# Performance work log

Measured on AMD Instinct MI355X. Metric: run time of the kernel, lower is better.

The kernel has to match this reference:

```python
import jax, jax.numpy as jnp
import numpy as np
import math

D_MODEL = 512
NUM_HEADS = 8
D_K = D_MODEL // NUM_HEADS
MAX_LEN = 500
BATCH = 32
SEQ = 480


def setup_inputs() -> dict:
    key = jax.random.key(0)
    ks = jax.random.split(key, 10)
    s = 0.02
    x = jax.random.normal(ks[0], (BATCH, SEQ, D_MODEL), dtype=jnp.float32)
    wq = jax.random.normal(ks[1], (D_MODEL, D_MODEL), dtype=jnp.float32) * s
    bq = jnp.zeros((D_MODEL,), jnp.float32)
    wk = jax.random.normal(ks[2], (D_MODEL, D_MODEL), dtype=jnp.float32) * s
    bk = jnp.zeros((D_MODEL,), jnp.float32)
    wv = jax.random.normal(ks[3], (D_MODEL, D_MODEL), dtype=jnp.float32) * s
    bv = jnp.zeros((D_MODEL,), jnp.float32)
    wo = jax.random.normal(ks[4], (D_MODEL, D_MODEL), dtype=jnp.float32) * s
    bo = jnp.zeros((D_MODEL,), jnp.float32)
    rel_bias = jax.random.normal(ks[5], (NUM_HEADS, MAX_LEN, MAX_LEN), dtype=jnp.float32) * 0.02
    return {"x": x, "wq": wq, "bq": bq, "wk": wk, "bk": bk, "wv": wv,
            "bv": bv, "wo": wo, "bo": bo, "rel_bias": rel_bias}


def reference(x, wq, bq, wk, bk, wv, bv, wo, bo, rel_bias):
    B, S, D = x.shape
    H, dk = NUM_HEADS, D_K
    scale = math.sqrt(dk)
    # QKV projections -> [B, H, S, dk]
    q = (x @ wq + bq).reshape(B, S, H, dk).transpose(0, 2, 1, 3)
    k = (x @ wk + bk).reshape(B, S, H, dk).transpose(0, 2, 1, 3)
    v = (x @ wv + bv).reshape(B, S, H, dk).transpose(0, 2, 1, 3)
    scores = jnp.einsum('bhqd,bhkd->bhqk', q, k) / scale
    scores = scores + rel_bias[None, :, :S, :S]
    causal = jnp.triu(jnp.ones((S, S), dtype=bool), k=1)  # True where j > i
    scores = jnp.where(causal[None, None], -jnp.inf, scores)
    attn = jax.nn.softmax(scores, axis=-1)
    ctx = jnp.einsum('bhqk,bhkd->bhqd', attn, v)
    ctx = ctx.transpose(0, 2, 1, 3).reshape(B, S, D)
    out = ctx @ wo + bo
    return out, attn.mean(axis=1)
```

## Files before the change

### kernel.cpp

```cpp
#include <hip/hip_runtime.h>
#include <hip/hip_bf16.h>


typedef unsigned short ushort_t;
typedef __attribute__((ext_vector_type(8))) short short8;
typedef __attribute__((ext_vector_type(4))) float floatx4;
typedef __attribute__((ext_vector_type(2))) __fp16 half2v;

#define NB 32
#define NS 480
#define ND 512
#define NH 8
#define NDK 64
#define MAXLEN 500
#define PSTR 36
#define SCL 0.18033688f

__device__ __forceinline__ ushort_t f2bf(float f) {
  union { float f; unsigned u; } v; v.f = f;
  unsigned r = v.u + 0x7FFFu + ((v.u >> 16) & 1u);
  return (ushort_t)(r >> 16);
}

#define GLOAD_LDS16(g, l)                                                      \
  __builtin_amdgcn_global_load_lds(                                            \
      (const __attribute__((address_space(1))) void*)(g),                      \
      (__attribute__((address_space(3))) void*)(l), 16, 0, 0)

__global__ __launch_bounds__(256)
void cvt_xw(const float* __restrict__ x, const float* __restrict__ wq,
            const float* __restrict__ wk, const float* __restrict__ wv,
            const float* __restrict__ wo, ushort_t* __restrict__ xb,
            ushort_t* __restrict__ wqT, ushort_t* __restrict__ wkT,
            ushort_t* __restrict__ wvT, ushort_t* __restrict__ woT) {
  __shared__ float t[32][33];
  const int bid = blockIdx.x;
  if (bid < 7680) {
    int idx = bid * 256 + threadIdx.x;
    float4 v = ((const float4*)x)[idx];
    ushort4 o;
    o.x = f2bf(v.x); o.y = f2bf(v.y); o.z = f2bf(v.z); o.w = f2bf(v.w);
    ((ushort4*)xb)[idx] = o;
    return;
  }
  const int q = bid - 7680;
  const int z = q >> 8;
  const float* w = (z == 0) ? wq : (z == 1) ? wk : (z == 2) ? wv : wo;
  ushort_t* wT = (z == 0) ? wqT : (z == 1) ? wkT : (z == 2) ? wvT : woT;
  int k0 = (q & 15) * 32, n0 = ((q >> 4) & 15) * 32;
  int tx = threadIdx.x & 31, ty = threadIdx.x >> 5;
#pragma unroll
  for (int yy = 0; yy < 4; ++yy)
    t[ty + yy * 8][tx] = w[(k0 + ty + yy * 8) * ND + n0 + tx];
  __syncthreads();
#pragma unroll
  for (int yy = 0; yy < 4; ++yy)
    wT[(n0 + ty + yy * 8) * ND + k0 + tx] = f2bf(t[tx][ty + yy * 8]);
}

__global__ void cvt_rbt(const float* __restrict__ rel_bias, float* __restrict__ rbt) {
  int kt = blockIdx.x, ib = blockIdx.y, h = blockIdx.z;
  int lm = threadIdx.x & 15, ii = threadIdx.x >> 4;
  int i = ib * 16 + ii;
  float f0 = rel_bias[((size_t)h * MAXLEN + i) * MAXLEN + kt * 32 + lm] * 1.44269504f;
  float f1 = rel_bias[((size_t)h * MAXLEN + i) * MAXLEN + kt * 32 + 16 + lm] * 1.44269504f;
  float2 o = {f0, f1};
  *(float2*)&rbt[(((size_t)h * 15 + kt) * NS + i) * 32 + 2 * lm] = o;
}

__global__ __launch_bounds__(256)
void qkv_gemm(const ushort_t* __restrict__ xb,
              const ushort_t* __restrict__ wqT, const ushort_t* __restrict__ wkT,
              const ushort_t* __restrict__ wvT,
              const float* __restrict__ bq, const float* __restrict__ bk,
              const float* __restrict__ bv,
              ushort_t* __restrict__ qb, ushort_t* __restrict__ kb,
              ushort_t* __restrict__ vtil) {
  __shared__ __align__(16) ushort_t sA[128 * 64];
  __shared__ __align__(16) ushort_t sB[128 * 64];
  const int tid = threadIdx.x;
  const int wid = tid >> 6, lane = tid & 63;
  const int lm = lane & 15, quad = lane >> 4;
  const int wr = wid >> 1, wc = wid & 1;
  const int z = blockIdx.z;

  floatx4 zero4 = {0.f, 0.f, 0.f, 0.f};
  floatx4 acc[4][4];
#pragma unroll
  for (int i = 0; i < 4; ++i)
#pragma unroll
    for (int j = 0; j < 4; ++j) acc[i][j] = zero4;

  if (z < 2) {
    if (blockIdx.x >= 120) return;
    const int row0 = blockIdx.x * 128;
    const int col0 = blockIdx.y * 128;
    const ushort_t* Bt = (z == 0) ? wqT : wkT;
    const float* bias = (z == 0) ? bq : bk;

    for (int k0 = 0; k0 < ND; k0 += 64) {
#pragma unroll
      for (int c = 0; c < 4; ++c) {
        int li = c * 256 + tid;
        int row = li >> 3, kc = li & 7;
        int kcs = kc ^ (row & 7);
        GLOAD_LDS16(xb + (row0 + row) * ND + k0 + kcs * 8, sA + (c * 256 + wid * 64) * 8);
        GLOAD_LDS16(Bt + (col0 + row) * ND + k0 + kcs * 8, sB + (c * 256 + wid * 64) * 8);
      }
      __syncthreads();
#pragma unroll
      for (int h2 = 0; h2 < 2; ++h2) {
        short8 a[4], b[4];
#pragma unroll
        for (int i = 0; i < 4; ++i) {
          int row = wr * 64 + i * 16 + lm;
          a[i] = *(const short8*)&sA[row * 64 + (((h2 << 2) | quad) ^ (lm & 7)) * 8];
        }
#pragma unroll
        for (int j = 0; j < 4; ++j) {
          int row = wc * 64 + j * 16 + lm;
          b[j] = *(const short8*)&sB[row * 64 + (((h2 << 2) | quad) ^ (lm & 7)) * 8];
        }
#pragma unroll
        for (int i = 0; i < 4; ++i)
#pragma unroll
          for (int j = 0; j < 4; ++j)
            acc[i][j] = __builtin_amdgcn_mfma_f32_16x16x32_bf16(a[i], b[j], acc[i][j], 0, 0, 0);
      }
      __syncthreads();
    }

    float bsv[4];
#pragma unroll
    for (int j = 0; j < 4; ++j) bsv[j] = bias[col0 + wc * 64 + j * 16 + lm];

#pragma unroll
    for (int i = 0; i < 4; ++i)
#pragma unroll
      for (int j = 0; j < 4; ++j)
#pragma unroll
        for (int r = 0; r < 4; ++r) {
          int m = row0 + wr * 64 + i * 16 + quad * 4 + r;
          int n = col0 + wc * 64 + j * 16 + lm;
          float val = acc[i][j][r] + bsv[j];
          int bb = m / NS, s = m - bb * NS;
          int h = n >> 6, d = n & 63;
          ushort_t o = f2bf(val);
          if (z == 0) qb[((bb * NH + h) * NS + s) * NDK + d] = o;
          else        kb[((bb * NH + h) * NS + s) * NDK + d] = o;
        }
  } else {
    const int b = blockIdx.x >> 2;
    const int row0 = (blockIdx.x & 3) * 128;
    const int col0 = blockIdx.y * 128;
    const ushort_t* xbb = xb + (size_t)b * NS * ND;

    for (int k0 = 0; k0 < ND; k0 += 64) {
#pragma unroll
      for (int c = 0; c < 4; ++c) {
        int li = c * 256 + tid;
        int row = li >> 3, kc = li & 7;
        int kcs = kc ^ (row & 7);
        GLOAD_LDS16(wvT + (row0 + row) * ND + k0 + kcs * 8, sA + (c * 256 + wid * 64) * 8);
        int srow = min(col0 + row, NS - 1);
        GLOAD_LDS16(xbb + srow * ND + k0 + kcs * 8, sB + (c * 256 + wid * 64) * 8);
      }
      __syncthreads();
#pragma unroll
      for (int h2 = 0; h2 < 2; ++h2) {
        short8 a[4], b2[4];
#pragma unroll
        for (int i = 0; i < 4; ++i) {
          int row = wr * 64 + i * 16 + lm;
          a[i] = *(const short8*)&sA[row * 64 + (((h2 << 2) | quad) ^ (lm & 7)) * 8];
        }
#pragma unroll
        for (int j = 0; j < 4; ++j) {
          int row = wc * 64 + j * 16 + lm;
          b2[j] = *(const short8*)&sB[row * 64 + (((h2 << 2) | quad) ^ (lm & 7)) * 8];
        }
#pragma unroll
        for (int i = 0; i < 4; ++i)
#pragma unroll
          for (int j = 0; j < 4; ++j)
            acc[i][j] = __builtin_amdgcn_mfma_f32_16x16x32_bf16(a[i], b2[j], acc[i][j], 0, 0, 0);
      }
      __syncthreads();
    }

#pragma unroll
    for (int i = 0; i < 4; ++i)
#pragma unroll
      for (int r = 0; r < 4; ++r) {
        int m = row0 + wr * 64 + i * 16 + quad * 4 + r;
        float bias = bv[m];
#pragma unroll
        for (int j = 0; j < 4; ++j) {
          int n = col0 + wc * 64 + j * 16 + lm;
          if (n < NS) {
            size_t idx = (((size_t)b * NH + (m >> 6)) * 15 + (n >> 5)) * 2048 +
                         (m & 63) * 32 + (n & 31);
            vtil[idx] = f2bf(acc[i][j][r] + bias);
          }
        }
      }
  }
}

__global__ __launch_bounds__(256)
void flash_attn(const ushort_t* __restrict__ qb, const ushort_t* __restrict__ kb,
                const ushort_t* __restrict__ vtil, const float* __restrict__ rbt,
                ushort_t* __restrict__ ctxb, float* __restrict__ cst,
                uint4* __restrict__ pscr) {
  const int bh = blockIdx.x;
  const int b = bh >> 3, h = bh & 7;
  const int tid = threadIdx.x;
  const int wid = tid >> 6, lane = tid & 63;
  const int lm = lane & 15, quad = lane >> 4;

  __shared__ __align__(16) ushort_t sP[4][32 * PSTR];

  const int slot = blockIdx.y * 4 + wid;
  const int tA = (slot == 7) ? 14 : slot;
  const int tB = (slot == 7) ? -1 : 13 - slot;

  const ushort_t* qh = qb + (size_t)bh * NS * NDK;
  const ushort_t* kh = kb + (size_t)bh * NS * NDK;
  const ushort_t* vb = vtil + (size_t)bh * 15 * 2048;
  const float* rb = rbt + (size_t)h * 15 * NS * 32;

#pragma unroll 1
  for (int ti = 0; ti < 2; ++ti) {
    const int t = (ti == 0) ? tA : tB;
    if (t < 0) break;
    const int nkt = t + 1;
    uint4* pp = pscr + ((size_t)(bh * 120 + (t * (t + 1)) / 2)) * 128 + lane;

    short8 aq[2][2];
#pragma unroll
    for (int g = 0; g < 2; ++g) {
      aq[g][0] = *(const short8*)&qh[(t * 32 + g * 16 + lm) * NDK + quad * 8];
      aq[g][1] = *(const short8*)&qh[(t * 32 + g * 16 + lm) * NDK + 32 + quad * 8];
    }

    float lsum[2][4];
    floatx4 O[2][4];
    floatx4 zero4 = {0.f, 0.f, 0.f, 0.f};
#pragma unroll
    for (int g = 0; g < 2; ++g) {
#pragma unroll
      for (int r = 0; r < 4; ++r) lsum[g][r] = 0.f;
#pragma unroll
      for (int jd = 0; jd < 4; ++jd) O[g][jd] = zero4;
    }

    for (int kt = 0; kt < nkt; ++kt) {
      const int kvA = kt * 32 + lm;
      const int kvB = kvA + 16;
      short8 bkA0 = *(const short8*)&kh[kvA * NDK + quad * 8];
      short8 bkA1 = *(const short8*)&kh[kvA * NDK + 32 + quad * 8];
      short8 bkB0 = *(const short8*)&kh[kvB * NDK + quad * 8];
      short8 bkB1 = *(const short8*)&kh[kvB * NDK + 32 + quad * 8];
      short8 bv2[4];
#pragma unroll
      for (int jd = 0; jd < 4; ++jd)
        bv2[jd] = *(const short8*)&vb[kt * 2048 + (jd * 16 + lm) * 32 + quad * 8];
      float2 bb[2][4];
#pragma unroll
      for (int g = 0; g < 2; ++g)
#pragma unroll
        for (int r = 0; r < 4; ++r) {
          int i = t * 32 + g * 16 + quad * 4 + r;
          bb[g][r] = *(const float2*)&rb[((size_t)kt * NS + i) * 32 + 2 * lm];
        }

      floatx4 sA[2], sB[2];
      __builtin_amdgcn_s_setprio(1);
#pragma unroll
      for (int g = 0; g < 2; ++g) {
        floatx4 s = zero4;
        s = __builtin_amdgcn_mfma_f32_16x16x32_bf16(aq[g][0], bkA0, s, 0, 0, 0);
        s = __builtin_amdgcn_mfma_f32_16x16x32_bf16(aq[g][1], bkA1, s, 0, 0, 0);
        sA[g] = s;
        s = zero4;
        s = __builtin_amdgcn_mfma_f32_16x16x32_bf16(aq[g][0], bkB0, s, 0, 0, 0);
        s = __builtin_amdgcn_mfma_f32_16x16x32_bf16(aq[g][1], bkB1, s, 0, 0, 0);
        sB[g] = s;
      }
      __builtin_amdgcn_s_setprio(0);

      const bool diag = (kt == t);
#pragma unroll
      for (int g = 0; g < 2; ++g) {
        unsigned pw[4];
#pragma unroll
        for (int r = 0; r < 4; ++r) {
          float p0 = __builtin_amdgcn_exp2f(fmaf(sA[g][r], SCL, bb[g][r].x));
          float p1 = __builtin_amdgcn_exp2f(fmaf(sB[g][r], SCL, bb[g][r].y));
          if (diag) {
            int i = t * 32 + g * 16 + quad * 4 + r;
            if (kvA > i) p0 = 0.f;
            if (kvB > i) p1 = 0.f;
          }
          lsum[g][r] += p0 + p1;
          unsigned pk;
          asm("v_cvt_pk_bf16_f32 %0, %1, %2" : "=v"(pk) : "v"(p0), "v"(p1));
          sP[wid][(g * 16 + quad * 4 + r) * PSTR + lm] = (ushort_t)(pk & 0xffffu);
          sP[wid][(g * 16 + quad * 4 + r) * PSTR + 16 + lm] = (ushort_t)(pk >> 16);
          half2v hp = __builtin_amdgcn_cvt_pkrtz(p0, p1);
          pw[r] = *(unsigned*)&hp;
        }
        uint4 pq = {pw[0], pw[1], pw[2], pw[3]};
        pp[(size_t)kt * 128 + g * 64] = pq;
      }

      __builtin_amdgcn_s_setprio(1);
#pragma unroll
      for (int g = 0; g < 2; ++g) {
        short8 ap = *(const short8*)&sP[wid][(g * 16 + lm) * PSTR + quad * 8];
#pragma unroll
        for (int jd = 0; jd < 4; ++jd)
          O[g][jd] = __builtin_amdgcn_mfma_f32_16x16x32_bf16(ap, bv2[jd], O[g][jd], 0, 0, 0);
      }
      __builtin_amdgcn_s_setprio(0);
    }

#pragma unroll
    for (int off = 1; off < 16; off <<= 1)
#pragma unroll
      for (int g = 0; g < 2; ++g)
#pragma unroll
        for (int r = 0; r < 4; ++r) lsum[g][r] += __shfl_xor(lsum[g][r], off, 64);

#pragma unroll
    for (int g = 0; g < 2; ++g) {
      float rinv[4];
#pragma unroll
      for (int r = 0; r < 4; ++r) rinv[r] = 1.f / lsum[g][r];
#pragma unroll
      for (int jd = 0; jd < 4; ++jd)
#pragma unroll
        for (int r = 0; r < 4; ++r) {
          int i = t * 32 + g * 16 + quad * 4 + r;
          ctxb[((size_t)b * NS + i) * ND + h * NDK + jd * 16 + lm] =
              f2bf(O[g][jd][r] * rinv[r]);
        }
      if (lm == 0) {
#pragma unroll
        for (int r = 0; r < 4; ++r) {
          int i = t * 32 + g * 16 + quad * 4 + r;
          cst[(size_t)bh * NS + i] = rinv[r];
        }
      }
    }
  }
}

__global__ __launch_bounds__(64)
void attn_mean_p(const uint4* __restrict__ pscr, const float* __restrict__ cst,
                 float* __restrict__ am) {
  const int b = blockIdx.x, t = blockIdx.y, kt = blockIdx.z;
  const int lane = threadIdx.x;
  const int lm = lane & 15, quad = lane >> 4;
  float* outp = am + ((size_t)b * NS + t * 32) * NS + (size_t)kt * 32;
  if (kt > t) {
#pragma unroll
    for (int g = 0; g < 2; ++g)
#pragma unroll
      for (int r = 0; r < 4; ++r) {
        int row = g * 16 + quad * 4 + r;
        outp[(size_t)row * NS + lm] = 0.f;
        outp[(size_t)row * NS + 16 + lm] = 0.f;
      }
    return;
  }
  const int m = (t * (t + 1)) / 2 + kt;
  float a0[2][4], a1[2][4];
#pragma unroll
  for (int g = 0; g < 2; ++g)
#pragma unroll
    for (int r = 0; r < 4; ++r) { a0[g][r] = 0.f; a1[g][r] = 0.f; }

#pragma unroll
  for (int h = 0; h < NH; ++h) {
    const uint4* pp = pscr + ((size_t)(b * NH + h) * 120 + m) * 128 + lane;
    uint4 q0 = pp[0];
    uint4 q1 = pp[64];
    unsigned pu[8] = {q0.x, q0.y, q0.z, q0.w, q1.x, q1.y, q1.z, q1.w};
    const float* cp = cst + (size_t)(b * NH + h) * NS + t * 32 + quad * 4;
    float4 rv0 = *(const float4*)cp;
    float4 rv1 = *(const float4*)(cp + 16);
    float rv[8] = {rv0.x, rv0.y, rv0.z, rv0.w, rv1.x, rv1.y, rv1.z, rv1.w};
#pragma unroll
    for (int g = 0; g < 2; ++g)
#pragma unroll
      for (int r = 0; r < 4; ++r) {
        half2v hp = *(half2v*)&pu[g * 4 + r];
        a0[g][r] = fmaf((float)hp.x, rv[g * 4 + r], a0[g][r]);
        a1[g][r] = fmaf((float)hp.y, rv[g * 4 + r], a1[g][r]);
      }
  }

#pragma unroll
  for (int g = 0; g < 2; ++g)
#pragma unroll
    for (int r = 0; r < 4; ++r) {
      int row = g * 16 + quad * 4 + r;
      outp[(size_t)row * NS + lm] = a0[g][r] * 0.125f;
      outp[(size_t)row * NS + 16 + lm] = a1[g][r] * 0.125f;
    }
}

__global__ __launch_bounds__(256)
void out_gemm(const ushort_t* __restrict__ ctxb, const ushort_t* __restrict__ woT,
              const float* __restrict__ bo, float* __restrict__ out) {
  __shared__ __align__(16) ushort_t sA[128 * 64];
  __shared__ __align__(16) ushort_t sB[128 * 64];
  const int tid = threadIdx.x;
  const int wid = tid >> 6, lane = tid & 63;
  const int lm = lane & 15, quad = lane >> 4;
  const int wr = wid >> 1, wc = wid & 1;
  const int row0 = blockIdx.x * 128;
  const int col0 = blockIdx.y * 128;

  floatx4 zero4 = {0.f, 0.f, 0.f, 0.f};
  floatx4 acc[4][4];
#pragma unroll
  for (int i = 0; i < 4; ++i)
#pragma unroll
    for (int j = 0; j < 4; ++j) acc[i][j] = zero4;

  for (int k0 = 0; k0 < ND; k0 += 64) {
#pragma unroll
    for (int c = 0; c < 4; ++c) {
      int li = c * 256 + tid;
      int row = li >> 3, kc = li & 7;
      int kcs = kc ^ (row & 7);
      GLOAD_LDS16(ctxb + (row0 + row) * ND + k0 + kcs * 8, sA + (c * 256 + wid * 64) * 8);
      GLOAD_LDS16(woT + (col0 + row) * ND + k0 + kcs * 8, sB + (c * 256 + wid * 64) * 8);
    }
    __syncthreads();
#pragma unroll
    for (int h2 = 0; h2 < 2; ++h2) {
      short8 a[4], b[4];
#pragma unroll
      for (int i = 0; i < 4; ++i) {
        int row = wr * 64 + i * 16 + lm;
        a[i] = *(const short8*)&sA[row * 64 + (((h2 << 2) | quad) ^ (lm & 7)) * 8];
      }
#pragma unroll
      for (int j = 0; j < 4; ++j) {
        int row = wc * 64 + j * 16 + lm;
        b[j] = *(const short8*)&sB[row * 64 + (((h2 << 2) | quad) ^ (lm & 7)) * 8];
      }
#pragma unroll
      for (int i = 0; i < 4; ++i)
#pragma unroll
        for (int j = 0; j < 4; ++j)
          acc[i][j] = __builtin_amdgcn_mfma_f32_16x16x32_bf16(a[i], b[j], acc[i][j], 0, 0, 0);
    }
    __syncthreads();
  }

  float bsv[4];
#pragma unroll
  for (int j = 0; j < 4; ++j) bsv[j] = bo[col0 + wc * 64 + j * 16 + lm];

#pragma unroll
  for (int i = 0; i < 4; ++i)
#pragma unroll
    for (int j = 0; j < 4; ++j)
#pragma unroll
      for (int r = 0; r < 4; ++r) {
        int m = row0 + wr * 64 + i * 16 + quad * 4 + r;
        int n = col0 + wc * 64 + j * 16 + lm;
        out[m * ND + n] = acc[i][j][r] + bsv[j];
      }
}

extern "C" void kernel_launch(void* const* d_in, const int* in_sizes, int n_in,
                              void* d_out, int out_size, void* d_ws, size_t ws_size,
                              hipStream_t stream) {
  const float* x  = (const float*)d_in[0];
  const float* wq = (const float*)d_in[1];
  const float* bq = (const float*)d_in[2];
  const float* wk = (const float*)d_in[3];
  const float* bk = (const float*)d_in[4];
  const float* wv = (const float*)d_in[5];
  const float* bv = (const float*)d_in[6];
  const float* wo = (const float*)d_in[7];
  const float* bo = (const float*)d_in[8];
  const float* rel_bias = (const float*)d_in[9];

  char* w = (char*)d_ws;
  ushort_t* xb  = (ushort_t*)w;
  ushort_t* wqT = (ushort_t*)(w + 15728640);
  ushort_t* wkT = wqT + 262144;
  ushort_t* wvT = wkT + 262144;
  ushort_t* woT = wvT + 262144;
  ushort_t* qb  = (ushort_t*)(w + 15728640 + 4 * 524288);
  ushort_t* kb  = qb + 7864320;
  ushort_t* vtil = kb + 7864320;
  ushort_t* ctxb = vtil + 7864320;
  float* cstat = (float*)(w + 80740352);
  uint4* pscr = (uint4*)(w + 81264640);
  float* rbt = (float*)w;

  float* out0 = (float*)d_out;
  float* attn_mean = out0 + 7864320;

  cvt_xw<<<dim3(8704), dim3(256), 0, stream>>>(x, wq, wk, wv, wo, xb, wqT, wkT, wvT, woT);
  qkv_gemm<<<dim3(128, 4, 3), dim3(256), 0, stream>>>(xb, wqT, wkT, wvT, bq, bk, bv,
                                                      qb, kb, vtil);
  cvt_rbt<<<dim3(15, 30, 8), dim3(256), 0, stream>>>(rel_bias, rbt);
  flash_attn<<<dim3(256, 2), dim3(256), 0, stream>>>(qb, kb, vtil, rbt, ctxb, cstat, pscr);
  attn_mean_p<<<dim3(32, 15, 15), dim3(64), 0, stream>>>(pscr, cstat, attn_mean);
  out_gemm<<<dim3(120, 4), dim3(256), 0, stream>>>(ctxb, woT, bo, out0);
}
```

Before: 226.4 us.

## Double-buffer LDS tiles in QKV and output GEMMs to overlap loads with MFMA

Allocates two LDS buffers per operand in the QKV and output projection GEMMs. The global-to-LDS load of the next K tile is issued before computing on the current one, leaving one barrier per iteration. This is meant to hide global load latency behind MFMA work. It doubles LDS use per block to 64 KB, which may lower occupancy.

```diff
diff --git a/kernel.cpp b/kernel.cpp
--- a/kernel.cpp
+++ b/kernel.cpp
@@ -76,8 +76,8 @@
               const float* __restrict__ bv,
               ushort_t* __restrict__ qb, ushort_t* __restrict__ kb,
               ushort_t* __restrict__ vtil) {
-  __shared__ __align__(16) ushort_t sA[128 * 64];
-  __shared__ __align__(16) ushort_t sB[128 * 64];
+  __shared__ __align__(16) ushort_t sA[2][128 * 64];
+  __shared__ __align__(16) ushort_t sB[2][128 * 64];
   const int tid = threadIdx.x;
   const int wid = tid >> 6, lane = tid & 63;
   const int lm = lane & 15, quad = lane >> 4;
@@ -90,6 +90,9 @@
   for (int i = 0; i < 4; ++i)
 #pragma unroll
     for (int j = 0; j < 4; ++j) acc[i][j] = zero4;
+
+  const int srow_ = tid >> 3, skc = tid & 7;
+  const int skcs = skc ^ (srow_ & 7);
 
   if (z < 2) {
     if (blockIdx.x >= 120) return;
@@ -98,28 +101,39 @@
     const ushort_t* Bt = (z == 0) ? wqT : wkT;
     const float* bias = (z == 0) ? bq : bk;
 
-    for (int k0 = 0; k0 < ND; k0 += 64) {
-#pragma unroll
-      for (int c = 0; c < 4; ++c) {
-        int li = c * 256 + tid;
-        int row = li >> 3, kc = li & 7;
-        int kcs = kc ^ (row & 7);
-        GLOAD_LDS16(xb + (row0 + row) * ND + k0 + kcs * 8, sA + (c * 256 + wid * 64) * 8);
-        GLOAD_LDS16(Bt + (col0 + row) * ND + k0 + kcs * 8, sB + (c * 256 + wid * 64) * 8);
-      }
-      __syncthreads();
+#pragma unroll
+    for (int c = 0; c < 4; ++c) {
+      int row = c * 32 + srow_;
+      GLOAD_LDS16(xb + (row0 + row) * ND + skcs * 8, &sA[0][(c * 256 + wid * 64) * 8]);
+      GLOAD_LDS16(Bt + (col0 + row) * ND + skcs * 8, &sB[0][(c * 256 + wid * 64) * 8]);
+    }
+    __syncthreads();
+
+    int buf = 0;
+    for (int t = 0; t < 8; ++t) {
+      if (t < 7) {
+        int k0n = (t + 1) * 64;
+#pragma unroll
+        for (int c = 0; c < 4; ++c) {
+          int row = c * 32 + srow_;
+          GLOAD_LDS16(xb + (row0 + row) * ND + k0n + skcs * 8,
+                      &sA[buf ^ 1][(c * 256 + wid * 64) * 8]);
+          GLOAD_LDS16(Bt + (col0 + row) * ND + k0n + skcs * 8,
+                      &sB[buf ^ 1][(c * 256 + wid * 64) * 8]);
+        }
+      }
 #pragma unroll
       for (int h2 = 0; h2 < 2; ++h2) {
         short8 a[4], b[4];
 #pragma unroll
         for (int i = 0; i < 4; ++i) {
           int row = wr * 64 + i * 16 + lm;
-          a[i] = *(const short8*)&sA[row * 64 + (((h2 << 2) | quad) ^ (lm & 7)) * 8];
+          a[i] = *(const short8*)&sA[buf][row * 64 + (((h2 << 2) | quad) ^ (lm & 7)) * 8];
         }
 #pragma unroll
         for (int j = 0; j < 4; ++j) {
           int row = wc * 64 + j * 16 + lm;
-          b[j] = *(const short8*)&sB[row * 64 + (((h2 << 2) | quad) ^ (lm & 7)) * 8];
+          b[j] = *(const short8*)&sB[buf][row * 64 + (((h2 << 2) | quad) ^ (lm & 7)) * 8];
         }
 #pragma unroll
         for (int i = 0; i < 4; ++i)
@@ -128,6 +142,7 @@
             acc[i][j] = __builtin_amdgcn_mfma_f32_16x16x32_bf16(a[i], b[j], acc[i][j], 0, 0, 0);
       }
       __syncthreads();
+      buf ^= 1;
     }
 
     float bsv[4];
@@ -155,29 +170,41 @@
     const int col0 = blockIdx.y * 128;
     const ushort_t* xbb = xb + (size_t)b * NS * ND;
 
-    for (int k0 = 0; k0 < ND; k0 += 64) {
-#pragma unroll
-      for (int c = 0; c < 4; ++c) {
-        int li = c * 256 + tid;
-        int row = li >> 3, kc = li & 7;
-        int kcs = kc ^ (row & 7);
-        GLOAD_LDS16(wvT + (row0 + row) * ND + k0 + kcs * 8, sA + (c * 256 + wid * 64) * 8);
-        int srow = min(col0 + row, NS - 1);
-        GLOAD_LDS16(xbb + srow * ND + k0 + kcs * 8, sB + (c * 256 + wid * 64) * 8);
-      }
-      __syncthreads();
+#pragma unroll
+    for (int c = 0; c < 4; ++c) {
+      int row = c * 32 + srow_;
+      GLOAD_LDS16(wvT + (row0 + row) * ND + skcs * 8, &sA[0][(c * 256 + wid * 64) * 8]);
+      int sr = min(col0 + row, NS - 1);
+      GLOAD_LDS16(xbb + sr * ND + skcs * 8, &sB[0][(c * 256 + wid * 64) * 8]);
+    }
+    __syncthreads();
+
+    int buf = 0;
+    for (int t = 0; t < 8; ++t) {
+      if (t < 7) {
+        int k0n = (t + 1) * 64;
+#pragma unroll
+        for (int c = 0; c < 4; ++c) {
+          int row = c * 32 + srow_;
+          GLOAD_LDS16(wvT + (row0 + row) * ND + k0n + skcs * 8,
+                      &sA[buf ^ 1][(c * 256 + wid * 64) * 8]);
+          int sr = min(col0 + row, NS - 1);
+          GLOAD_LDS16(xbb + sr * ND + k0n + skcs * 8,
+                      &sB[buf ^ 1][(c * 256 + wid * 64) * 8]);
+        }
+      }
 #pragma unroll
       for (int h2 = 0; h2 < 2; ++h2) {
         short8 a[4], b2[4];
 #pragma unroll
         for (int i = 0; i < 4; ++i) {
           int row = wr * 64 + i * 16 + lm;
-          a[i] = *(const short8*)&sA[row * 64 + (((h2 << 2) | quad) ^ (lm & 7)) * 8];
+          a[i] = *(const short8*)&sA[buf][row * 64 + (((h2 << 2) | quad) ^ (lm & 7)) * 8];
         }
 #pragma unroll
         for (int j = 0; j < 4; ++j) {
           int row = wc * 64 + j * 16 + lm;
-          b2[j] = *(const short8*)&sB[row * 64 + (((h2 << 2) | quad) ^ (lm & 7)) * 8];
+          b2[j] = *(const short8*)&sB[buf][row * 64 + (((h2 << 2) | quad) ^ (lm & 7)) * 8];
         }
 #pragma unroll
         for (int i = 0; i < 4; ++i)
@@ -186,6 +213,7 @@
             acc[i][j] = __builtin_amdgcn_mfma_f32_16x16x32_bf16(a[i], b2[j], acc[i][j], 0, 0, 0);
       }
       __syncthreads();
+      buf ^= 1;
     }
 
 #pragma unroll
@@ -414,14 +442,16 @@
 __global__ __launch_bounds__(256)
 void out_gemm(const ushort_t* __restrict__ ctxb, const ushort_t* __restrict__ woT,
               const float* __restrict__ bo, float* __restrict__ out) {
-  __shared__ __align__(16) ushort_t sA[128 * 64];
-  __shared__ __align__(16) ushort_t sB[128 * 64];
+  __shared__ __align__(16) ushort_t sA[2][128 * 64];
+  __shared__ __align__(16) ushort_t sB[2][128 * 64];
   const int tid = threadIdx.x;
   const int wid = tid >> 6, lane = tid & 63;
   const int lm = lane & 15, quad = lane >> 4;
   const int wr = wid >> 1, wc = wid & 1;
   const int row0 = blockIdx.x * 128;
   const int col0 = blockIdx.y * 128;
+  const int srow_ = tid >> 3, skc = tid & 7;
+  const int skcs = skc ^ (srow_ & 7);
 
   floatx4 zero4 = {0.f, 0.f, 0.f, 0.f};
   floatx4 acc[4][4];
@@ -430,28 +460,39 @@
 #pragma unroll
     for (int j = 0; j < 4; ++j) acc[i][j] = zero4;
 
-  for (int k0 = 0; k0 < ND; k0 += 64) {
-#pragma unroll
-    for (int c = 0; c < 4; ++c) {
-      int li = c * 256 + tid;
-      int row = li >> 3, kc = li & 7;
-      int kcs = kc ^ (row & 7);
-      GLOAD_LDS16(ctxb + (row0 + row) * ND + k0 + kcs * 8, sA + (c * 256 + wid * 64) * 8);
-      GLOAD_LDS16(woT + (col0 + row) * ND + k0 + kcs * 8, sB + (c * 256 + wid * 64) * 8);
-    }
-    __syncthreads();
+#pragma unroll
+  for (int c = 0; c < 4; ++c) {
+    int row = c * 32 + srow_;
+    GLOAD_LDS16(ctxb + (row0 + row) * ND + skcs * 8, &sA[0][(c * 256 + wid * 64) * 8]);
+    GLOAD_LDS16(woT + (col0 + row) * ND + skcs * 8, &sB[0][(c * 256 + wid * 64) * 8]);
+  }
+  __syncthreads();
+
+  int buf = 0;
+  for (int t = 0; t < 8; ++t) {
+    if (t < 7) {
+      int k0n = (t + 1) * 64;
+#pragma unroll
+      for (int c = 0; c < 4; ++c) {
+        int row = c * 32 + srow_;
+        GLOAD_LDS16(ctxb + (row0 + row) * ND + k0n + skcs * 8,
+                    &sA[buf ^ 1][(c * 256 + wid * 64) * 8]);
+        GLOAD_LDS16(woT + (col0 + row) * ND + k0n + skcs * 8,
+                    &sB[buf ^ 1][(c * 256 + wid * 64) * 8]);
+      }
+    }
 #pragma unroll
     for (int h2 = 0; h2 < 2; ++h2) {
       short8 a[4], b[4];
 #pragma unroll
       for (int i = 0; i < 4; ++i) {
         int row = wr * 64 + i * 16 + lm;
-        a[i] = *(const short8*)&sA[row * 64 + (((h2 << 2) | quad) ^ (lm & 7)) * 8];
+        a[i] = *(const short8*)&sA[buf][row * 64 + (((h2 << 2) | quad) ^ (lm & 7)) * 8];
       }
 #pragma unroll
       for (int j = 0; j < 4; ++j) {
         int row = wc * 64 + j * 16 + lm;
-        b[j] = *(const short8*)&sB[row * 64 + (((h2 << 2) | quad) ^ (lm & 7)) * 8];
+        b[j] = *(const short8*)&sB[buf][row * 64 + (((h2 << 2) | quad) ^ (lm & 7)) * 8];
       }
 #pragma unroll
       for (int i = 0; i < 4; ++i)
@@ -460,6 +501,7 @@
           acc[i][j] = __builtin_amdgcn_mfma_f32_16x16x32_bf16(a[i], b[j], acc[i][j], 0, 0, 0);
     }
     __syncthreads();
+    buf ^= 1;
   }
 
   float bsv[4];
```

After: 220.9 us, median of 3. 1.03x faster.
